# Optimization experiments

Measured on AMD Instinct MI355X. Metric: run time of the kernel, lower is better.

The kernel has to match this reference:

```python
import jax, jax.numpy as jnp
import numpy as np

N, E, D, ED, G = 50000, 600000, 128, 32, 64
NEG_SLOPE = 0.2

def layer_norm(x, g, b, eps=1e-5):
    mu = jnp.mean(x, axis=-1, keepdims=True)
    var = jnp.var(x, axis=-1, keepdims=True)
    return (x - mu) * jax.lax.rsqrt(var + eps) * g + b

def eagat(x, src, dst, edge_attr, W, a_src, a_dst, We, a_e, bias):
    # GATConv with edge features, heads=1; messages flow src -> dst
    xl = x @ W                               # [N, D]
    ee = edge_attr @ We                      # [E, D]
    al_s = xl @ a_src                        # [N]
    al_d = xl @ a_dst                        # [N]
    e = jax.nn.leaky_relu(al_s[src] + al_d[dst] + ee @ a_e, NEG_SLOPE)  # [E]
    # segment softmax over incoming edges of each dst node
    m = jax.ops.segment_max(e, dst, num_segments=N)
    ex = jnp.exp(e - m[dst])
    s = jax.ops.segment_sum(ex, dst, num_segments=N)
    alpha = ex / (s[dst] + 1e-16)            # [E]
    out = jax.ops.segment_sum(xl[src] * alpha[:, None], dst, num_segments=N)
    return out + bias

def setup_inputs() -> dict:
    key = jax.random.key(0)
    ks = jax.random.split(key, 24)
    p = lambda k, shp, sc=0.1: jax.random.normal(k, shp, dtype=jnp.float32) * sc
    inp = {
        "x": jax.random.normal(ks[0], (N, D), dtype=jnp.float32),
        "edge_attr": jax.random.normal(ks[1], (E, ED), dtype=jnp.float32),
        "W1": p(ks[2], (D, D)), "as1": p(ks[3], (D,)), "ad1": p(ks[4], (D,)),
        "We1": p(ks[5], (ED, D)), "ae1": p(ks[6], (D,)), "b1": jnp.zeros((D,), jnp.float32),
        "g1": jnp.ones((D,), jnp.float32), "be1": jnp.zeros((D,), jnp.float32),
        "W2": p(ks[7], (D, D)), "as2": p(ks[8], (D,)), "ad2": p(ks[9], (D,)),
        "We2": p(ks[10], (ED, D)), "ae2": p(ks[11], (D,)), "b2": jnp.zeros((D,), jnp.float32),
        "g2": jnp.ones((D,), jnp.float32), "be2": jnp.zeros((D,), jnp.float32),
        "Wl": p(ks[12], (D, D)), "bl": jnp.zeros((D,), jnp.float32),
        "gl": jnp.ones((D,), jnp.float32), "bel": jnp.zeros((D,), jnp.float32),
        "edge_index": jax.random.randint(ks[13], (2, E), 0, N, dtype=jnp.int64),
        "batch": jnp.sort(jax.random.randint(ks[14], (N,), 0, G, dtype=jnp.int64)),
    }
    return inp

def reference(x, edge_attr, W1, as1, ad1, We1, ae1, b1, g1, be1,
              W2, as2, ad2, We2, ae2, b2, g2, be2, Wl, bl, gl, bel,
              edge_index, batch):
    src, dst = edge_index[0], edge_index[1]
    x1 = eagat(x, src, dst, edge_attr, W1, as1, ad1, We1, ae1, b1)
    x2 = layer_norm(x1, g1, be1)
    x3 = eagat(x2, src, dst, edge_attr, W2, as2, ad2, We2, ae2, b2)
    x4 = layer_norm(x3, g2, be2)
    # global mean pool over graphs
    sums = jax.ops.segment_sum(x4, batch, num_segments=G)          # [G, D]
    cnt = jax.ops.segment_sum(jnp.ones((x4.shape[0],), x4.dtype), batch, num_segments=G)
    pooled = sums / jnp.maximum(cnt, 1.0)[:, None]
    out = jax.nn.relu(layer_norm(pooled @ Wl + bl, gl, bel))
    return out
```

## Files before the change

kernel.cpp:

```cpp
#include <hip/hip_runtime.h>
#include <math.h>


typedef __attribute__((ext_vector_type(8))) short bf16x8;
typedef __attribute__((ext_vector_type(4))) float f32x4;

static __device__ __forceinline__ unsigned short f2bf(float f) {
    unsigned u = __float_as_uint(f);
    unsigned r = (u + 0x7fff + ((u >> 16) & 1)) >> 16;
    return (unsigned short)r;
}

__global__ __launch_bounds__(64) void prep_wa(
    const float* __restrict__ We1, const float* __restrict__ ae1,
    const float* __restrict__ We2, const float* __restrict__ ae2,
    float* __restrict__ wa )
{
    int t = threadIdx.x;
    const float* We = (t < 32) ? We1 : We2;
    const float* ae = (t < 32) ? ae1 : ae2;
    int r = t & 31;
    float s = 0.f;
    for (int c = 0; c < 128; c++) s += We[r*128 + c] * ae[c];
    wa[t] = s;
}

__global__ __launch_bounds__(256) void prep_wb(
    const float* __restrict__ W1, const float* __restrict__ W2,
    unsigned short* __restrict__ W1bT, unsigned short* __restrict__ W2bT)
{
    int i = blockIdx.x * 256 + threadIdx.x;
    int k = i >> 7, n = i & 127;
    W1bT[n * 128 + k] = f2bf(W1[i]);
    W2bT[n * 128 + k] = f2bf(W2[i]);
}

__global__ __launch_bounds__(256) void edge_dots_count(
    const float* __restrict__ ea, const float* __restrict__ wa,
    const int* __restrict__ dstv,
    float* __restrict__ edot1, float* __restrict__ edot2,
    int* __restrict__ counts, int E)
{
    int j = blockIdx.x * 256 + threadIdx.x;
    if (j >= E) return;
    const float4* e4 = (const float4*)(ea + (size_t)j * 32);
    float s1 = 0.f, s2 = 0.f;
#pragma unroll
    for (int i = 0; i < 8; i++) {
        float4 v = e4[i];
        float4 w1 = ((const float4*)wa)[i];
        float4 w2 = ((const float4*)(wa + 32))[i];
        s1 += v.x*w1.x + v.y*w1.y + v.z*w1.z + v.w*w1.w;
        s2 += v.x*w2.x + v.y*w2.y + v.z*w2.z + v.w*w2.w;
    }
    edot1[j] = s1; edot2[j] = s2;
    atomicAdd(&counts[dstv[j]], 1);
}

__global__ __launch_bounds__(256) void gemm_mfma(
    const float* __restrict__ X, const unsigned short* __restrict__ WbT,
    const float* __restrict__ asrc, const float* __restrict__ adst,
    unsigned short* __restrict__ XLb, float* __restrict__ als, float* __restrict__ ald,
    int nrows)
{
    int t = threadIdx.x;
    int wave = t >> 6;
    int lane = t & 63;
    int l = lane & 15, q = lane >> 4;
    int row0 = blockIdx.x * 64 + wave * 16;

    int arow = row0 + l;
    bool avalid = arow < nrows;
    const float* xrow = X + (size_t)arow * 128 + q * 8;

    f32x4 acc[8];
#pragma unroll
    for (int c = 0; c < 8; c++) acc[c] = (f32x4){0.f, 0.f, 0.f, 0.f};

#pragma unroll
    for (int kt = 0; kt < 4; kt++) {
        bf16x8 afrag;
        if (avalid) {
            float4 v0 = *(const float4*)(xrow + kt * 32);
            float4 v1 = *(const float4*)(xrow + kt * 32 + 4);
            afrag[0] = (short)f2bf(v0.x); afrag[1] = (short)f2bf(v0.y);
            afrag[2] = (short)f2bf(v0.z); afrag[3] = (short)f2bf(v0.w);
            afrag[4] = (short)f2bf(v1.x); afrag[5] = (short)f2bf(v1.y);
            afrag[6] = (short)f2bf(v1.z); afrag[7] = (short)f2bf(v1.w);
        } else {
#pragma unroll
            for (int j = 0; j < 8; j++) afrag[j] = 0;
        }
#pragma unroll
        for (int c = 0; c < 8; c++) {
            bf16x8 bfrag = *(const bf16x8*)(WbT + (((c * 16 + l) << 7) + kt * 32 + q * 8));
            acc[c] = __builtin_amdgcn_mfma_f32_16x16x32_bf16(afrag, bfrag, acc[c], 0, 0, 0);
        }
    }

    float as_[8], ad_[8];
#pragma unroll
    for (int c = 0; c < 8; c++) { as_[c] = asrc[c * 16 + l]; ad_[c] = adst[c * 16 + l]; }

#pragma unroll
    for (int r = 0; r < 4; r++) {
        int row = row0 + q * 4 + r;
        bool valid = row < nrows;
        float ps = 0.f, pd = 0.f;
#pragma unroll
        for (int c = 0; c < 8; c++) {
            float v = acc[c][r];
            if (valid) XLb[(size_t)row * 128 + c * 16 + l] = f2bf(v);
            ps += v * as_[c]; pd += v * ad_[c];
        }
#pragma unroll
        for (int o = 8; o >= 1; o >>= 1) { ps += __shfl_xor(ps, o); pd += __shfl_xor(pd, o); }
        if (l == 0 && valid) { als[row] = ps; ald[row] = pd; }
    }
}

__global__ __launch_bounds__(256) void edge_logits(
    const float* __restrict__ edot, const int* __restrict__ srcv, const int* __restrict__ dstv,
    const int* __restrict__ rank,
    const float* __restrict__ als, const float* __restrict__ ald,
    float* __restrict__ elogc, int E)
{
    int j = blockIdx.x * 256 + threadIdx.x;
    if (j >= E) return;
    float s = edot[j] + als[srcv[j]] + ald[dstv[j]];
    elogc[rank[j]] = (s >= 0.f) ? s : 0.2f * s;
}

__global__ __launch_bounds__(256) void scan_local(
    const int* __restrict__ counts, int* __restrict__ local,
    int* __restrict__ bsums, int n)
{
    __shared__ int tmp[256];
    int b = blockIdx.x, t = threadIdx.x;
    int base = b * 1024 + t * 4;
    int v0 = 0, v1 = 0, v2 = 0, v3 = 0;
    if (base + 3 < n) {
        const int4 c4 = *(const int4*)(counts + base);
        v0 = c4.x; v1 = c4.y; v2 = c4.z; v3 = c4.w;
    } else {
        if (base + 0 < n) v0 = counts[base + 0];
        if (base + 1 < n) v1 = counts[base + 1];
        if (base + 2 < n) v2 = counts[base + 2];
        if (base + 3 < n) v3 = counts[base + 3];
    }
    tmp[t] = v0 + v1 + v2 + v3; __syncthreads();
    for (int o = 1; o < 256; o <<= 1) {
        int x = (t >= o) ? tmp[t - o] : 0;
        __syncthreads();
        tmp[t] += x;
        __syncthreads();
    }
    int run = (t == 0) ? 0 : tmp[t - 1];
    if (base + 0 < n) { local[base + 0] = run; run += v0; }
    if (base + 1 < n) { local[base + 1] = run; run += v1; }
    if (base + 2 < n) { local[base + 2] = run; run += v2; }
    if (base + 3 < n) { local[base + 3] = run; }
    if (t == 255) bsums[b] = tmp[255];
}

__global__ __launch_bounds__(256) void scan_bsums(int* __restrict__ bsums, int nb)
{
    __shared__ int tmp[256];
    int t = threadIdx.x;
    tmp[t] = (t < nb) ? bsums[t] : 0; __syncthreads();
    for (int o = 1; o < 256; o <<= 1) {
        int x = (t >= o) ? tmp[t - o] : 0;
        __syncthreads();
        tmp[t] += x;
        __syncthreads();
    }
    if (t < nb) bsums[t] = (t == 0) ? 0 : tmp[t - 1];
}

__global__ __launch_bounds__(256) void scan_add(
    const int* __restrict__ local, const int* __restrict__ bsums,
    int* __restrict__ offs, int* __restrict__ cursor, int n, int E)
{
    int i = blockIdx.x * 256 + threadIdx.x;
    if (i < n) {
        int v = local[i] + bsums[i >> 10];
        offs[i] = v; cursor[i] = v;
    }
    if (i == 0) offs[n] = E;
}

__global__ __launch_bounds__(256) void scatter_edges(
    const int* __restrict__ srcv, const int* __restrict__ dstv,
    int* __restrict__ cursor, int* __restrict__ srcc, int* __restrict__ rank, int E)
{
    int j = blockIdx.x * 256 + threadIdx.x;
    if (j < E) {
        int p = atomicAdd(&cursor[dstv[j]], 1);
        srcc[p] = srcv[j];
        rank[j] = p;
    }
}

__global__ __launch_bounds__(256) void aggregate_ln(
    const unsigned short* __restrict__ XLb, const float* __restrict__ elogc,
    const int* __restrict__ offs, const int* __restrict__ srcc,
    const float* __restrict__ bias, const float* __restrict__ gamma, const float* __restrict__ beta,
    float* __restrict__ Xout, int N)
{
    int node = blockIdx.x * 4 + (threadIdx.x >> 6);
    if (node >= N) return;
    int lane = threadIdx.x & 63;
    int lo = offs[node], hi = offs[node + 1];
    int deg = hi - lo;

    float mloc = -3.402823466e38f;
    for (int j = lane; j < deg; j += 64) mloc = fmaxf(mloc, elogc[lo + j]);
#pragma unroll
    for (int o = 32; o >= 1; o >>= 1) mloc = fmaxf(mloc, __shfl_xor(mloc, o));
    float m = mloc;

    const unsigned* rows = (const unsigned*)XLb;
    float acc0 = 0.f, acc1 = 0.f, ssum = 0.f;
    int j = 0;
    for (; j + 4 <= deg; j += 4) {
        int   s0 = srcc[lo + j],     s1 = srcc[lo + j + 1];
        int   s2 = srcc[lo + j + 2], s3 = srcc[lo + j + 3];
        float e0 = elogc[lo + j],     e1 = elogc[lo + j + 1];
        float e2 = elogc[lo + j + 2], e3 = elogc[lo + j + 3];
        unsigned u0 = rows[((size_t)s0 << 6) + lane];
        unsigned u1 = rows[((size_t)s1 << 6) + lane];
        unsigned u2 = rows[((size_t)s2 << 6) + lane];
        unsigned u3 = rows[((size_t)s3 << 6) + lane];
        float w0 = __expf(e0 - m), w1 = __expf(e1 - m);
        float w2 = __expf(e2 - m), w3 = __expf(e3 - m);
        ssum += (w0 + w1) + (w2 + w3);
        acc0 += w0 * __uint_as_float(u0 << 16);
        acc1 += w0 * __uint_as_float(u0 & 0xffff0000u);
        acc0 += w1 * __uint_as_float(u1 << 16);
        acc1 += w1 * __uint_as_float(u1 & 0xffff0000u);
        acc0 += w2 * __uint_as_float(u2 << 16);
        acc1 += w2 * __uint_as_float(u2 & 0xffff0000u);
        acc0 += w3 * __uint_as_float(u3 << 16);
        acc1 += w3 * __uint_as_float(u3 & 0xffff0000u);
    }
    for (; j < deg; j++) {
        int   s0 = srcc[lo + j];
        float w0 = __expf(elogc[lo + j] - m);
        unsigned u0 = rows[((size_t)s0 << 6) + lane];
        ssum += w0;
        acc0 += w0 * __uint_as_float(u0 << 16);
        acc1 += w0 * __uint_as_float(u0 & 0xffff0000u);
    }

    float2 bi = *(const float2*)(bias + 2 * lane);
    float inv = 1.f / (ssum + 1e-16f);
    float y0 = acc0 * inv + bi.x;
    float y1 = acc1 * inv + bi.y;

    float s = y0 + y1;
#pragma unroll
    for (int o = 32; o >= 1; o >>= 1) s += __shfl_xor(s, o);
    float mean = s * (1.f / 128.f);
    float d0 = y0 - mean, d1 = y1 - mean;
    float v = d0 * d0 + d1 * d1;
#pragma unroll
    for (int o = 32; o >= 1; o >>= 1) v += __shfl_xor(v, o);
    float r = rsqrtf(v * (1.f / 128.f) + 1e-5f);
    float2 ga = *(const float2*)(gamma + 2 * lane);
    float2 be = *(const float2*)(beta  + 2 * lane);
    float2 o2;
    o2.x = d0 * r * ga.x + be.x;
    o2.y = d1 * r * ga.y + be.y;
    *(float2*)(Xout + (size_t)node * 128 + 2 * lane) = o2;
}

__global__ __launch_bounds__(128) void pool_partial(
    const float* __restrict__ X4, const int* __restrict__ batch,
    float* __restrict__ pooled, int n)
{
    int chunk0 = blockIdx.x * 64;
    if (chunk0 >= n) return;
    int t = threadIdx.x;
    int end = min(chunk0 + 64, n);
    float acc = 0.f;
    int gcur = batch[chunk0];
    for (int r = chunk0; r < end; r++) {
        int g = batch[r];
        if (g != gcur) {
            atomicAdd(&pooled[gcur * 128 + t], acc);
            acc = 0.f; gcur = g;
        }
        acc += X4[(size_t)r * 128 + t];
    }
    atomicAdd(&pooled[gcur * 128 + t], acc);
}

__global__ __launch_bounds__(128) void pool_head(
    const float* __restrict__ pooled, const int* __restrict__ batch,
    const float* __restrict__ Wl, const float* __restrict__ bl,
    const float* __restrict__ gl, const float* __restrict__ bel,
    float* __restrict__ out, int n)
{
    int g = blockIdx.x, t = threadIdx.x;
    int lo = 0, hi = n;
    while (lo < hi) { int mid = (lo + hi) >> 1; if (batch[mid] < g) lo = mid + 1; else hi = mid; }
    int s = lo;
    hi = n;
    while (lo < hi) { int mid = (lo + hi) >> 1; if (batch[mid] < g + 1) lo = mid + 1; else hi = mid; }
    float cntf = (float)(lo - s);

    __shared__ float ps[128];
    __shared__ float red[128];
    ps[t] = pooled[g * 128 + t] / fmaxf(cntf, 1.f);
    __syncthreads();

    float y = bl[t];
    for (int k = 0; k < 128; k++) y += ps[k] * Wl[k * 128 + t];

    red[t] = y; __syncthreads();
#pragma unroll
    for (int o = 64; o >= 1; o >>= 1) { if (t < o) red[t] += red[t + o]; __syncthreads(); }
    float mean = red[0] * (1.f / 128.f); __syncthreads();
    float d = y - mean;
    red[t] = d * d; __syncthreads();
#pragma unroll
    for (int o = 64; o >= 1; o >>= 1) { if (t < o) red[t] += red[t + o]; __syncthreads(); }
    float var = red[0] * (1.f / 128.f);
    float z = d * rsqrtf(var + 1e-5f) * gl[t] + bel[t];
    out[g * 128 + t] = fmaxf(z, 0.f);
}


extern "C" void kernel_launch(void* const* d_in, const int* in_sizes, int n_in,
                              void* d_out, int out_size, void* d_ws, size_t ws_size,
                              hipStream_t stream)
{
    const float* x    = (const float*)d_in[0];
    const float* ea   = (const float*)d_in[1];
    const float* W1   = (const float*)d_in[2];
    const float* as1  = (const float*)d_in[3];
    const float* ad1  = (const float*)d_in[4];
    const float* We1  = (const float*)d_in[5];
    const float* ae1  = (const float*)d_in[6];
    const float* b1   = (const float*)d_in[7];
    const float* g1   = (const float*)d_in[8];
    const float* be1  = (const float*)d_in[9];
    const float* W2   = (const float*)d_in[10];
    const float* as2  = (const float*)d_in[11];
    const float* ad2  = (const float*)d_in[12];
    const float* We2  = (const float*)d_in[13];
    const float* ae2  = (const float*)d_in[14];
    const float* b2   = (const float*)d_in[15];
    const float* g2   = (const float*)d_in[16];
    const float* be2  = (const float*)d_in[17];
    const float* Wlin = (const float*)d_in[18];
    const float* bl   = (const float*)d_in[19];
    const float* gl   = (const float*)d_in[20];
    const float* bel  = (const float*)d_in[21];
    const int*   ei   = (const int*)d_in[22];
    const int*   batch= (const int*)d_in[23];
    float* out = (float*)d_out;

    int N = in_sizes[0] / 128;
    int E = in_sizes[1] / 32;
    int G = out_size / 128;
    const int* srcv = ei;
    const int* dstv = ei + E;

    char* wsb = (char*)d_ws;
    size_t off = 0;
    auto alloc = [&](size_t bytes) -> void* {
        void* p = wsb + off;
        off += (bytes + 15) & ~(size_t)15;
        return p;
    };
    unsigned short* XLb  = (unsigned short*)alloc((size_t)N * 128 * 2);
    unsigned short* W1bT = (unsigned short*)alloc(16384 * 2);
    unsigned short* W2bT = (unsigned short*)alloc(16384 * 2);
    float* XA     = (float*)alloc((size_t)N * 128 * 4);
    float* elogc  = (float*)alloc((size_t)E * 4);
    float* edot1  = (float*)alloc((size_t)E * 4);
    float* edot2  = (float*)alloc((size_t)E * 4);
    float* als    = (float*)alloc((size_t)N * 4);
    float* ald    = (float*)alloc((size_t)N * 4);
    float* wa     = (float*)alloc(64 * 4);
    float* pooled = (float*)alloc((size_t)G * 128 * 4);
    int*   counts = (int*)alloc((size_t)N * 4);
    int*   local  = (int*)alloc((size_t)N * 4);
    int*   bsums  = (int*)alloc(256 * 4);
    int*   offs   = (int*)alloc((size_t)(N + 1) * 4);
    int*   cursor = (int*)alloc((size_t)N * 4);
    int*   srcc   = (int*)alloc((size_t)E * 4);
    int*   rank   = (int*)alloc((size_t)E * 4);

    int egrid = (E + 255) / 256;
    int mgrid = (N + 63) / 64;
    int agrid = (N + 3) / 4;
    int pgrid = (N + 63) / 64;
    int sgrid = (N + 1023) / 1024;
    int ngrid = (N + 255) / 256;

    hipMemsetAsync(counts, 0, (size_t)N * 4, stream);
    hipMemsetAsync(pooled, 0, (size_t)G * 128 * 4, stream);
    prep_wa<<<1, 64, 0, stream>>>(We1, ae1, We2, ae2, wa);
    prep_wb<<<64, 256, 0, stream>>>(W1, W2, W1bT, W2bT);
    edge_dots_count<<<egrid, 256, 0, stream>>>(ea, wa, dstv, edot1, edot2, counts, E);
    scan_local<<<sgrid, 256, 0, stream>>>(counts, local, bsums, N);
    scan_bsums<<<1, 256, 0, stream>>>(bsums, sgrid);
    scan_add<<<ngrid, 256, 0, stream>>>(local, bsums, offs, cursor, N, E);
    scatter_edges<<<egrid, 256, 0, stream>>>(srcv, dstv, cursor, srcc, rank, E);

    gemm_mfma<<<mgrid, 256, 0, stream>>>(x, W1bT, as1, ad1, XLb, als, ald, N);
    edge_logits<<<egrid, 256, 0, stream>>>(edot1, srcv, dstv, rank, als, ald, elogc, E);
    aggregate_ln<<<agrid, 256, 0, stream>>>(XLb, elogc, offs, srcc, b1, g1, be1, XA, N);

    gemm_mfma<<<mgrid, 256, 0, stream>>>(XA, W2bT, as2, ad2, XLb, als, ald, N);
    edge_logits<<<egrid, 256, 0, stream>>>(edot2, srcv, dstv, rank, als, ald, elogc, E);
    aggregate_ln<<<agrid, 256, 0, stream>>>(XLb, elogc, offs, srcc, b2, g2, be2, XA, N);

    pool_partial<<<pgrid, 128, 0, stream>>>(XA, batch, pooled, N);
    pool_head<<<G, 128, 0, stream>>>(pooled, batch, Wlin, bl, gl, bel, out, N);
}
```

Measured before the change: 407.4 us.

## Fuse edge logits into aggregation, store intermediates in bf16, merge small kernels

Edge logit computation moves into the aggregation kernel: the edge dot products are permuted into CSR order during the scatter, and each wave computes its node's logits from als/ald, with a shuffle-based path for degree ≤64. This removes the edge_logits kernels and the rank array. Layer outputs are stored in bf16 and the second GEMM reads them directly, halving that traffic at some extra precision loss. The weight-prep kernels are merged into one, as are the two scan-fixup kernels.

```diff
diff --git a/kernel.cpp b/kernel.cpp
--- a/kernel.cpp
+++ b/kernel.cpp
@@ -10,29 +10,30 @@
     unsigned r = (u + 0x7fff + ((u >> 16) & 1)) >> 16;
     return (unsigned short)r;
 }
-
-__global__ __launch_bounds__(64) void prep_wa(
+static __device__ __forceinline__ float bf2f_lo(unsigned u) { return __uint_as_float(u << 16); }
+static __device__ __forceinline__ float bf2f_hi(unsigned u) { return __uint_as_float(u & 0xffff0000u); }
+
+__global__ __launch_bounds__(256) void prep_weights(
+    const float* __restrict__ W1, const float* __restrict__ W2,
     const float* __restrict__ We1, const float* __restrict__ ae1,
     const float* __restrict__ We2, const float* __restrict__ ae2,
+    unsigned short* __restrict__ W1bT, unsigned short* __restrict__ W2bT,
     float* __restrict__ wa )
 {
-    int t = threadIdx.x;
-    const float* We = (t < 32) ? We1 : We2;
-    const float* ae = (t < 32) ? ae1 : ae2;
-    int r = t & 31;
-    float s = 0.f;
-    for (int c = 0; c < 128; c++) s += We[r*128 + c] * ae[c];
-    wa[t] = s;
-}
-
-__global__ __launch_bounds__(256) void prep_wb(
-    const float* __restrict__ W1, const float* __restrict__ W2,
-    unsigned short* __restrict__ W1bT, unsigned short* __restrict__ W2bT)
-{
-    int i = blockIdx.x * 256 + threadIdx.x;
-    int k = i >> 7, n = i & 127;
-    W1bT[n * 128 + k] = f2bf(W1[i]);
-    W2bT[n * 128 + k] = f2bf(W2[i]);
+    int b = blockIdx.x, t = threadIdx.x;
+    if (b < 64) {
+        int i = b * 256 + t;
+        int k = i >> 7, n = i & 127;
+        W1bT[n * 128 + k] = f2bf(W1[i]);
+        W2bT[n * 128 + k] = f2bf(W2[i]);
+    } else if (t < 64) {
+        const float* We = (t < 32) ? We1 : We2;
+        const float* ae = (t < 32) ? ae1 : ae2;
+        int r = t & 31;
+        float s = 0.f;
+        for (int c = 0; c < 128; c++) s += We[r*128 + c] * ae[c];
+        wa[t] = s;
+    }
 }
 
 __global__ __launch_bounds__(256) void edge_dots_count(
@@ -55,80 +56,6 @@
     }
     edot1[j] = s1; edot2[j] = s2;
     atomicAdd(&counts[dstv[j]], 1);
-}
-
-__global__ __launch_bounds__(256) void gemm_mfma(
-    const float* __restrict__ X, const unsigned short* __restrict__ WbT,
-    const float* __restrict__ asrc, const float* __restrict__ adst,
-    unsigned short* __restrict__ XLb, float* __restrict__ als, float* __restrict__ ald,
-    int nrows)
-{
-    int t = threadIdx.x;
-    int wave = t >> 6;
-    int lane = t & 63;
-    int l = lane & 15, q = lane >> 4;
-    int row0 = blockIdx.x * 64 + wave * 16;
-
-    int arow = row0 + l;
-    bool avalid = arow < nrows;
-    const float* xrow = X + (size_t)arow * 128 + q * 8;
-
-    f32x4 acc[8];
-#pragma unroll
-    for (int c = 0; c < 8; c++) acc[c] = (f32x4){0.f, 0.f, 0.f, 0.f};
-
-#pragma unroll
-    for (int kt = 0; kt < 4; kt++) {
-        bf16x8 afrag;
-        if (avalid) {
-            float4 v0 = *(const float4*)(xrow + kt * 32);
-            float4 v1 = *(const float4*)(xrow + kt * 32 + 4);
-            afrag[0] = (short)f2bf(v0.x); afrag[1] = (short)f2bf(v0.y);
-            afrag[2] = (short)f2bf(v0.z); afrag[3] = (short)f2bf(v0.w);
-            afrag[4] = (short)f2bf(v1.x); afrag[5] = (short)f2bf(v1.y);
-            afrag[6] = (short)f2bf(v1.z); afrag[7] = (short)f2bf(v1.w);
-        } else {
-#pragma unroll
-            for (int j = 0; j < 8; j++) afrag[j] = 0;
-        }
-#pragma unroll
-        for (int c = 0; c < 8; c++) {
-            bf16x8 bfrag = *(const bf16x8*)(WbT + (((c * 16 + l) << 7) + kt * 32 + q * 8));
-            acc[c] = __builtin_amdgcn_mfma_f32_16x16x32_bf16(afrag, bfrag, acc[c], 0, 0, 0);
-        }
-    }
-
-    float as_[8], ad_[8];
-#pragma unroll
-    for (int c = 0; c < 8; c++) { as_[c] = asrc[c * 16 + l]; ad_[c] = adst[c * 16 + l]; }
-
-#pragma unroll
-    for (int r = 0; r < 4; r++) {
-        int row = row0 + q * 4 + r;
-        bool valid = row < nrows;
-        float ps = 0.f, pd = 0.f;
-#pragma unroll
-        for (int c = 0; c < 8; c++) {
-            float v = acc[c][r];
-            if (valid) XLb[(size_t)row * 128 + c * 16 + l] = f2bf(v);
-            ps += v * as_[c]; pd += v * ad_[c];
-        }
-#pragma unroll
-        for (int o = 8; o >= 1; o >>= 1) { ps += __shfl_xor(ps, o); pd += __shfl_xor(pd, o); }
-        if (l == 0 && valid) { als[row] = ps; ald[row] = pd; }
-    }
-}
-
-__global__ __launch_bounds__(256) void edge_logits(
-    const float* __restrict__ edot, const int* __restrict__ srcv, const int* __restrict__ dstv,
-    const int* __restrict__ rank,
-    const float* __restrict__ als, const float* __restrict__ ald,
-    float* __restrict__ elogc, int E)
-{
-    int j = blockIdx.x * 256 + threadIdx.x;
-    if (j >= E) return;
-    float s = edot[j] + als[srcv[j]] + ald[dstv[j]];
-    elogc[rank[j]] = (s >= 0.f) ? s : 0.2f * s;
 }
 
 __global__ __launch_bounds__(256) void scan_local(
@@ -163,7 +90,9 @@
     if (t == 255) bsums[b] = tmp[255];
 }
 
-__global__ __launch_bounds__(256) void scan_bsums(int* __restrict__ bsums, int nb)
+__global__ __launch_bounds__(256) void scan_add(
+    const int* __restrict__ local, const int* __restrict__ bsums,
+    int* __restrict__ offs, int* __restrict__ cursor, int n, int E, int nb)
 {
     __shared__ int tmp[256];
     int t = threadIdx.x;
@@ -174,16 +103,11 @@
         tmp[t] += x;
         __syncthreads();
     }
-    if (t < nb) bsums[t] = (t == 0) ? 0 : tmp[t - 1];
-}
-
-__global__ __launch_bounds__(256) void scan_add(
-    const int* __restrict__ local, const int* __restrict__ bsums,
-    int* __restrict__ offs, int* __restrict__ cursor, int n, int E)
-{
-    int i = blockIdx.x * 256 + threadIdx.x;
+    int i = blockIdx.x * 256 + t;
     if (i < n) {
-        int v = local[i] + bsums[i >> 10];
+        int blk = i >> 10;
+        int boff = (blk == 0) ? 0 : tmp[blk - 1];
+        int v = local[i] + boff;
         offs[i] = v; cursor[i] = v;
     }
     if (i == 0) offs[n] = E;
@@ -191,65 +115,185 @@
 
 __global__ __launch_bounds__(256) void scatter_edges(
     const int* __restrict__ srcv, const int* __restrict__ dstv,
-    int* __restrict__ cursor, int* __restrict__ srcc, int* __restrict__ rank, int E)
+    const float* __restrict__ edot1, const float* __restrict__ edot2,
+    int* __restrict__ cursor, int* __restrict__ srcc,
+    float* __restrict__ edotc1, float* __restrict__ edotc2, int E)
 {
     int j = blockIdx.x * 256 + threadIdx.x;
     if (j < E) {
         int p = atomicAdd(&cursor[dstv[j]], 1);
-        srcc[p] = srcv[j];
-        rank[j] = p;
+        srcc[p]   = srcv[j];
+        edotc1[p] = edot1[j];
+        edotc2[p] = edot2[j];
+    }
+}
+
+template<bool BF16IN>
+__global__ __launch_bounds__(256) void gemm_mfma(
+    const void* __restrict__ Xv, const unsigned short* __restrict__ WbT,
+    const float* __restrict__ asrc, const float* __restrict__ adst,
+    unsigned short* __restrict__ XLb, float* __restrict__ als, float* __restrict__ ald,
+    int nrows)
+{
+    int t = threadIdx.x;
+    int wave = t >> 6;
+    int lane = t & 63;
+    int l = lane & 15, q = lane >> 4;
+    int row0 = blockIdx.x * 64 + wave * 16;
+
+    int arow = row0 + l;
+    bool avalid = arow < nrows;
+
+    f32x4 acc[8];
+#pragma unroll
+    for (int c = 0; c < 8; c++) acc[c] = (f32x4){0.f, 0.f, 0.f, 0.f};
+
+#pragma unroll
+    for (int kt = 0; kt < 4; kt++) {
+        bf16x8 afrag;
+        if (avalid) {
+            if constexpr (BF16IN) {
+                const unsigned short* xrow = (const unsigned short*)Xv + (size_t)arow * 128 + q * 8;
+                afrag = *(const bf16x8*)(xrow + kt * 32);
+            } else {
+                const float* xrow = (const float*)Xv + (size_t)arow * 128 + q * 8;
+                float4 v0 = *(const float4*)(xrow + kt * 32);
+                float4 v1 = *(const float4*)(xrow + kt * 32 + 4);
+                afrag[0] = (short)f2bf(v0.x); afrag[1] = (short)f2bf(v0.y);
+                afrag[2] = (short)f2bf(v0.z); afrag[3] = (short)f2bf(v0.w);
+                afrag[4] = (short)f2bf(v1.x); afrag[5] = (short)f2bf(v1.y);
+                afrag[6] = (short)f2bf(v1.z); afrag[7] = (short)f2bf(v1.w);
+            }
+        } else {
+#pragma unroll
+            for (int j = 0; j < 8; j++) afrag[j] = 0;
+        }
+#pragma unroll
+        for (int c = 0; c < 8; c++) {
+            bf16x8 bfrag = *(const bf16x8*)(WbT + (((c * 16 + l) << 7) + kt * 32 + q * 8));
+            acc[c] = __builtin_amdgcn_mfma_f32_16x16x32_bf16(afrag, bfrag, acc[c], 0, 0, 0);
+        }
+    }
+
+    float as_[8], ad_[8];
+#pragma unroll
+    for (int c = 0; c < 8; c++) { as_[c] = asrc[c * 16 + l]; ad_[c] = adst[c * 16 + l]; }
+
+#pragma unroll
+    for (int r = 0; r < 4; r++) {
+        int row = row0 + q * 4 + r;
+        bool valid = row < nrows;
+        float ps = 0.f, pd = 0.f;
+#pragma unroll
+        for (int c = 0; c < 8; c++) {
+            float v = acc[c][r];
+            if (valid) XLb[(size_t)row * 128 + c * 16 + l] = f2bf(v);
+            ps += v * as_[c]; pd += v * ad_[c];
+        }
+#pragma unroll
+        for (int o = 8; o >= 1; o >>= 1) { ps += __shfl_xor(ps, o); pd += __shfl_xor(pd, o); }
+        if (l == 0 && valid) { als[row] = ps; ald[row] = pd; }
     }
 }
 
 __global__ __launch_bounds__(256) void aggregate_ln(
-    const unsigned short* __restrict__ XLb, const float* __restrict__ elogc,
+    const unsigned short* __restrict__ XLb, const float* __restrict__ edotc,
     const int* __restrict__ offs, const int* __restrict__ srcc,
+    const float* __restrict__ als, const float* __restrict__ ald,
     const float* __restrict__ bias, const float* __restrict__ gamma, const float* __restrict__ beta,
-    float* __restrict__ Xout, int N)
+    unsigned short* __restrict__ XoutB, int N)
 {
     int node = blockIdx.x * 4 + (threadIdx.x >> 6);
     if (node >= N) return;
     int lane = threadIdx.x & 63;
     int lo = offs[node], hi = offs[node + 1];
     int deg = hi - lo;
-
-    float mloc = -3.402823466e38f;
-    for (int j = lane; j < deg; j += 64) mloc = fmaxf(mloc, elogc[lo + j]);
-#pragma unroll
-    for (int o = 32; o >= 1; o >>= 1) mloc = fmaxf(mloc, __shfl_xor(mloc, o));
-    float m = mloc;
+    float ald_n = ald[node];
 
     const unsigned* rows = (const unsigned*)XLb;
     float acc0 = 0.f, acc1 = 0.f, ssum = 0.f;
-    int j = 0;
-    for (; j + 4 <= deg; j += 4) {
-        int   s0 = srcc[lo + j],     s1 = srcc[lo + j + 1];
-        int   s2 = srcc[lo + j + 2], s3 = srcc[lo + j + 3];
-        float e0 = elogc[lo + j],     e1 = elogc[lo + j + 1];
-        float e2 = elogc[lo + j + 2], e3 = elogc[lo + j + 3];
-        unsigned u0 = rows[((size_t)s0 << 6) + lane];
-        unsigned u1 = rows[((size_t)s1 << 6) + lane];
-        unsigned u2 = rows[((size_t)s2 << 6) + lane];
-        unsigned u3 = rows[((size_t)s3 << 6) + lane];
-        float w0 = __expf(e0 - m), w1 = __expf(e1 - m);
-        float w2 = __expf(e2 - m), w3 = __expf(e3 - m);
-        ssum += (w0 + w1) + (w2 + w3);
-        acc0 += w0 * __uint_as_float(u0 << 16);
-        acc1 += w0 * __uint_as_float(u0 & 0xffff0000u);
-        acc0 += w1 * __uint_as_float(u1 << 16);
-        acc1 += w1 * __uint_as_float(u1 & 0xffff0000u);
-        acc0 += w2 * __uint_as_float(u2 << 16);
-        acc1 += w2 * __uint_as_float(u2 & 0xffff0000u);
-        acc0 += w3 * __uint_as_float(u3 << 16);
-        acc1 += w3 * __uint_as_float(u3 & 0xffff0000u);
-    }
-    for (; j < deg; j++) {
-        int   s0 = srcc[lo + j];
-        float w0 = __expf(elogc[lo + j] - m);
-        unsigned u0 = rows[((size_t)s0 << 6) + lane];
-        ssum += w0;
-        acc0 += w0 * __uint_as_float(u0 << 16);
-        acc1 += w0 * __uint_as_float(u0 & 0xffff0000u);
+
+    if (deg <= 64) {
+        float e_mine = -3.402823466e38f;
+        int   s_mine = 0;
+        if (lane < deg) {
+            int p = lo + lane;
+            s_mine = srcc[p];
+            float e = edotc[p] + als[s_mine] + ald_n;
+            e_mine = (e >= 0.f) ? e : 0.2f * e;
+        }
+        float m = e_mine;
+#pragma unroll
+        for (int o = 32; o >= 1; o >>= 1) m = fmaxf(m, __shfl_xor(m, o));
+
+        int j = 0;
+        for (; j + 8 <= deg; j += 8) {
+            int s0=__shfl(s_mine,j),   s1=__shfl(s_mine,j+1), s2=__shfl(s_mine,j+2), s3=__shfl(s_mine,j+3);
+            int s4=__shfl(s_mine,j+4), s5=__shfl(s_mine,j+5), s6=__shfl(s_mine,j+6), s7=__shfl(s_mine,j+7);
+            unsigned u0 = rows[((size_t)s0 << 6) + lane];
+            unsigned u1 = rows[((size_t)s1 << 6) + lane];
+            unsigned u2 = rows[((size_t)s2 << 6) + lane];
+            unsigned u3 = rows[((size_t)s3 << 6) + lane];
+            unsigned u4 = rows[((size_t)s4 << 6) + lane];
+            unsigned u5 = rows[((size_t)s5 << 6) + lane];
+            unsigned u6 = rows[((size_t)s6 << 6) + lane];
+            unsigned u7 = rows[((size_t)s7 << 6) + lane];
+            float w0=__expf(__shfl(e_mine,j)-m),   w1=__expf(__shfl(e_mine,j+1)-m);
+            float w2=__expf(__shfl(e_mine,j+2)-m), w3=__expf(__shfl(e_mine,j+3)-m);
+            float w4=__expf(__shfl(e_mine,j+4)-m), w5=__expf(__shfl(e_mine,j+5)-m);
+            float w6=__expf(__shfl(e_mine,j+6)-m), w7=__expf(__shfl(e_mine,j+7)-m);
+            ssum += ((w0+w1)+(w2+w3)) + ((w4+w5)+(w6+w7));
+            acc0 += w0*bf2f_lo(u0); acc1 += w0*bf2f_hi(u0);
+            acc0 += w1*bf2f_lo(u1); acc1 += w1*bf2f_hi(u1);
+            acc0 += w2*bf2f_lo(u2); acc1 += w2*bf2f_hi(u2);
+            acc0 += w3*bf2f_lo(u3); acc1 += w3*bf2f_hi(u3);
+            acc0 += w4*bf2f_lo(u4); acc1 += w4*bf2f_hi(u4);
+            acc0 += w5*bf2f_lo(u5); acc1 += w5*bf2f_hi(u5);
+            acc0 += w6*bf2f_lo(u6); acc1 += w6*bf2f_hi(u6);
+            acc0 += w7*bf2f_lo(u7); acc1 += w7*bf2f_hi(u7);
+        }
+        for (; j + 4 <= deg; j += 4) {
+            int s0=__shfl(s_mine,j), s1=__shfl(s_mine,j+1), s2=__shfl(s_mine,j+2), s3=__shfl(s_mine,j+3);
+            unsigned u0 = rows[((size_t)s0 << 6) + lane];
+            unsigned u1 = rows[((size_t)s1 << 6) + lane];
+            unsigned u2 = rows[((size_t)s2 << 6) + lane];
+            unsigned u3 = rows[((size_t)s3 << 6) + lane];
+            float w0=__expf(__shfl(e_mine,j)-m),   w1=__expf(__shfl(e_mine,j+1)-m);
+            float w2=__expf(__shfl(e_mine,j+2)-m), w3=__expf(__shfl(e_mine,j+3)-m);
+            ssum += (w0+w1)+(w2+w3);
+            acc0 += w0*bf2f_lo(u0); acc1 += w0*bf2f_hi(u0);
+            acc0 += w1*bf2f_lo(u1); acc1 += w1*bf2f_hi(u1);
+            acc0 += w2*bf2f_lo(u2); acc1 += w2*bf2f_hi(u2);
+            acc0 += w3*bf2f_lo(u3); acc1 += w3*bf2f_hi(u3);
+        }
+        for (; j < deg; j++) {
+            int s0 = __shfl(s_mine, j);
+            float w0 = __expf(__shfl(e_mine, j) - m);
+            unsigned u0 = rows[((size_t)s0 << 6) + lane];
+            ssum += w0;
+            acc0 += w0*bf2f_lo(u0); acc1 += w0*bf2f_hi(u0);
+        }
+    } else {
+        float mloc = -3.402823466e38f;
+        for (int j = lane; j < deg; j += 64) {
+            int p = lo + j;
+            float e = edotc[p] + als[srcc[p]] + ald_n;
+            e = (e >= 0.f) ? e : 0.2f * e;
+            mloc = fmaxf(mloc, e);
+        }
+#pragma unroll
+        for (int o = 32; o >= 1; o >>= 1) mloc = fmaxf(mloc, __shfl_xor(mloc, o));
+        float m = mloc;
+        for (int j = 0; j < deg; j++) {
+            int p = lo + j;
+            int s0 = srcc[p];
+            float e = edotc[p] + als[s0] + ald_n;
+            e = (e >= 0.f) ? e : 0.2f * e;
+            float w = __expf(e - m);
+            unsigned u0 = rows[((size_t)s0 << 6) + lane];
+            ssum += w;
+            acc0 += w*bf2f_lo(u0); acc1 += w*bf2f_hi(u0);
+        }
     }
 
     float2 bi = *(const float2*)(bias + 2 * lane);
@@ -268,14 +312,14 @@
     float r = rsqrtf(v * (1.f / 128.f) + 1e-5f);
     float2 ga = *(const float2*)(gamma + 2 * lane);
     float2 be = *(const float2*)(beta  + 2 * lane);
-    float2 o2;
-    o2.x = d0 * r * ga.x + be.x;
-    o2.y = d1 * r * ga.y + be.y;
-    *(float2*)(Xout + (size_t)node * 128 + 2 * lane) = o2;
+    float o0 = d0 * r * ga.x + be.x;
+    float o1 = d1 * r * ga.y + be.y;
+    unsigned packed = (unsigned)f2bf(o0) | ((unsigned)f2bf(o1) << 16);
+    ((unsigned*)XoutB)[((size_t)node << 6) + lane] = packed;
 }
 
 __global__ __launch_bounds__(128) void pool_partial(
-    const float* __restrict__ X4, const int* __restrict__ batch,
+    const unsigned short* __restrict__ XAb, const int* __restrict__ batch,
     float* __restrict__ pooled, int n)
 {
     int chunk0 = blockIdx.x * 64;
@@ -290,7 +334,7 @@
             atomicAdd(&pooled[gcur * 128 + t], acc);
             acc = 0.f; gcur = g;
         }
-        acc += X4[(size_t)r * 128 + t];
+        acc += __uint_as_float(((unsigned)XAb[(size_t)r * 128 + t]) << 16);
     }
     atomicAdd(&pooled[gcur * 128 + t], acc);
 }
@@ -375,12 +419,13 @@
         return p;
     };
     unsigned short* XLb  = (unsigned short*)alloc((size_t)N * 128 * 2);
+    unsigned short* XAb  = (unsigned short*)alloc((size_t)N * 128 * 2);
     unsigned short* W1bT = (unsigned short*)alloc(16384 * 2);
     unsigned short* W2bT = (unsigned short*)alloc(16384 * 2);
-    float* XA     = (float*)alloc((size_t)N * 128 * 4);
-    float* elogc  = (float*)alloc((size_t)E * 4);
     float* edot1  = (float*)alloc((size_t)E * 4);
     float* edot2  = (float*)alloc((size_t)E * 4);
+    float* edotc1 = (float*)alloc((size_t)E * 4);
+    float* edotc2 = (float*)alloc((size_t)E * 4);
     float* als    = (float*)alloc((size_t)N * 4);
     float* ald    = (float*)alloc((size_t)N * 4);
     float* wa     = (float*)alloc(64 * 4);
@@ -391,7 +436,6 @@
     int*   offs   = (int*)alloc((size_t)(N + 1) * 4);
     int*   cursor = (int*)alloc((size_t)N * 4);
     int*   srcc   = (int*)alloc((size_t)E * 4);
-    int*   rank   = (int*)alloc((size_t)E * 4);
 
     int egrid = (E + 255) / 256;
     int mgrid = (N + 63) / 64;
@@ -402,22 +446,18 @@
 
     hipMemsetAsync(counts, 0, (size_t)N * 4, stream);
     hipMemsetAsync(pooled, 0, (size_t)G * 128 * 4, stream);
-    prep_wa<<<1, 64, 0, stream>>>(We1, ae1, We2, ae2, wa);
-    prep_wb<<<64, 256, 0, stream>>>(W1, W2, W1bT, W2bT);
+    prep_weights<<<65, 256, 0, stream>>>(W1, W2, We1, ae1, We2, ae2, W1bT, W2bT, wa);
     edge_dots_count<<<egrid, 256, 0, stream>>>(ea, wa, dstv, edot1, edot2, counts, E);
     scan_local<<<sgrid, 256, 0, stream>>>(counts, local, bsums, N);
-    scan_bsums<<<1, 256, 0, stream>>>(bsums, sgrid);
-    scan_add<<<ngrid, 256, 0, stream>>>(local, bsums, offs, cursor, N, E);
-    scatter_edges<<<egrid, 256, 0, stream>>>(srcv, dstv, cursor, srcc, rank, E);
-
-    gemm_mfma<<<mgrid, 256, 0, stream>>>(x, W1bT, as1, ad1, XLb, als, ald, N);
-    edge_logits<<<egrid, 256, 0, stream>>>(edot1, srcv, dstv, rank, als, ald, elogc, E);
-    aggregate_ln<<<agrid, 256, 0, stream>>>(XLb, elogc, offs, srcc, b1, g1, be1, XA, N);
-
-    gemm_mfma<<<mgrid, 256, 0, stream>>>(XA, W2bT, as2, ad2, XLb, als, ald, N);
-    edge_logits<<<egrid, 256, 0, stream>>>(edot2, srcv, dstv, rank, als, ald, elogc, E);
-    aggregate_ln<<<agrid, 256, 0, stream>>>(XLb, elogc, offs, srcc, b2, g2, be2, XA, N);
-
-    pool_partial<<<pgrid, 128, 0, stream>>>(XA, batch, pooled, N);
+    scan_add<<<ngrid, 256, 0, stream>>>(local, bsums, offs, cursor, N, E, sgrid);
+    scatter_edges<<<egrid, 256, 0, stream>>>(srcv, dstv, edot1, edot2, cursor, srcc, edotc1, edotc2, E);
+
+    gemm_mfma<false><<<mgrid, 256, 0, stream>>>(x, W1bT, as1, ad1, XLb, als, ald, N);
+    aggregate_ln<<<agrid, 256, 0, stream>>>(XLb, edotc1, offs, srcc, als, ald, b1, g1, be1, XAb, N);
+
+    gemm_mfma<true><<<mgrid, 256, 0, stream>>>(XAb, W2bT, as2, ad2, XLb, als, ald, N);
+    aggregate_ln<<<agrid, 256, 0, stream>>>(XLb, edotc2, offs, srcc, als, ald, b2, g2, be2, XAb, N);
+
+    pool_partial<<<pgrid, 128, 0, stream>>>(XAb, batch, pooled, N);
     pool_head<<<G, 128, 0, stream>>>(pooled, batch, Wlin, bl, gl, bel, out, N);
 }
```

After: 391.0 us. 1.04x faster.
